# Performance work log

Measured on AMD Instinct MI355X. Metric: run time of the kernel, lower is better.

The kernel has to match this reference:

```python
import jax, jax.numpy as jnp
from jax import lax
import numpy as np

C_IN, H, W = 9, 11, 11
N_FILT = 64
N_LAYERS = 8
FC_UNITS = 64
LSTM_H = 64
N_ACTIONS = 6
B, T = 32, 128


def setup_inputs() -> dict:
    key = jax.random.key(0)
    ks = jax.random.split(key, 24)
    s = 0.05
    d = {}
    d['x'] = jax.random.normal(ks[0], (B, T, C_IN, H, W), dtype=jnp.float32)
    d['conv0_w'] = jax.random.normal(ks[1], (N_FILT, C_IN, 3, 3), dtype=jnp.float32) * s
    d['conv0_b'] = jnp.zeros((N_FILT,), jnp.float32)
    d['conv_ws'] = jax.random.normal(ks[2], (N_LAYERS - 1, N_FILT, N_FILT, 3, 3), dtype=jnp.float32) * s
    d['conv_bs'] = jnp.zeros((N_LAYERS - 1, N_FILT), jnp.float32)
    d['fc_w'] = jax.random.normal(ks[3], (FC_UNITS, N_FILT * H * W), dtype=jnp.float32) * s
    d['fc_b'] = jnp.zeros((FC_UNITS,), jnp.float32)
    d['w_ih'] = jax.random.normal(ks[4], (4 * LSTM_H, FC_UNITS), dtype=jnp.float32) * s
    d['w_hh'] = jax.random.normal(ks[5], (4 * LSTM_H, LSTM_H), dtype=jnp.float32) * s
    d['b_ih'] = jnp.zeros((4 * LSTM_H,), jnp.float32)
    d['b_hh'] = jnp.zeros((4 * LSTM_H,), jnp.float32)
    d['p1_w'] = jax.random.normal(ks[6], (128, LSTM_H), dtype=jnp.float32) * s
    d['p1_b'] = jnp.zeros((128,), jnp.float32)
    d['p2_w'] = jax.random.normal(ks[7], (N_ACTIONS, 128), dtype=jnp.float32) * s
    d['p2_b'] = jnp.zeros((N_ACTIONS,), jnp.float32)
    d['v1_w'] = jax.random.normal(ks[8], (128, LSTM_H), dtype=jnp.float32) * s
    d['v1_b'] = jnp.zeros((128,), jnp.float32)
    d['v2_w'] = jax.random.normal(ks[9], (1, 128), dtype=jnp.float32) * s
    d['v2_b'] = jnp.zeros((1,), jnp.float32)
    return d


def _conv_relu(h, w, b):
    # h: [N, C, H, W], w: [O, I, 3, 3] -> SAME padding, stride 1
    y = lax.conv_general_dilated(h, w, (1, 1), [(1, 1), (1, 1)],
                                 dimension_numbers=('NCHW', 'OIHW', 'NCHW'))
    return jax.nn.relu(y + b[None, :, None, None])


def _forward(x, conv0_w, conv0_b, conv_ws, conv_bs, fc_w, fc_b,
             w_ih, w_hh, b_ih, b_hh, p1_w, p1_b, p2_w, p2_b, v1_w, v1_b, v2_w, v2_b):
    b, t = x.shape[0], x.shape[1]
    h = x.reshape(b * t, C_IN, H, W)          # batch CNN over all frames at once
    h = _conv_relu(h, conv0_w, conv0_b)
    for i in range(N_LAYERS - 1):             # fixed small layer loop
        h = _conv_relu(h, conv_ws[i], conv_bs[i])
    h = h.reshape(b * t, N_FILT * H * W)
    feats = jax.nn.relu(h @ fc_w.T + fc_b)    # [B*T, FC_UNITS]
    feats = feats.reshape(b, t, FC_UNITS)

    # LSTM (PyTorch gate order i, f, g, o)
    def step(carry, xt):
        hprev, cprev = carry
        g = xt @ w_ih.T + hprev @ w_hh.T + b_ih + b_hh
        i_g, f_g, g_g, o_g = jnp.split(g, 4, axis=-1)
        c = jax.nn.sigmoid(f_g) * cprev + jax.nn.sigmoid(i_g) * jnp.tanh(g_g)
        hn = jax.nn.sigmoid(o_g) * jnp.tanh(c)
        return (hn, c), hn

    h0 = jnp.zeros((b, LSTM_H), feats.dtype)
    c0 = jnp.zeros((b, LSTM_H), feats.dtype)
    _, outs = lax.scan(step, (h0, c0), jnp.swapaxes(feats, 0, 1))  # [T, B, H]
    lstm_out = jnp.swapaxes(outs, 0, 1)       # [B, T, H]

    p = jax.nn.relu(lstm_out @ p1_w.T + p1_b) @ p2_w.T + p2_b  # [B, T, n_actions]
    v = jax.nn.relu(lstm_out @ v1_w.T + v1_b) @ v2_w.T + v2_b  # [B, T, 1]
    return p, v


def reference(x, conv0_w, conv0_b, conv_ws, conv_bs, fc_w, fc_b,
              w_ih, w_hh, b_ih, b_hh, p1_w, p1_b, p2_w, p2_b, v1_w, v1_b, v2_w, v2_b):
    return _forward(x, conv0_w, conv0_b, conv_ws, conv_bs, fc_w, fc_b,
                    w_ih, w_hh, b_ih, b_hh, p1_w, p1_b, p2_w, p2_b,
                    v1_w, v1_b, v2_w, v2_b)
```

## Files before the change

kernel.cpp:

```cpp
#include <hip/hip_runtime.h>
#include <hip/hip_bf16.h>

typedef __attribute__((ext_vector_type(8))) short short8;
typedef __attribute__((ext_vector_type(4))) short short4_t;
typedef __attribute__((ext_vector_type(4))) float floatx4;
typedef __attribute__((ext_vector_type(16))) float floatx16;

#define MFMA_B16(a,b,c) __builtin_amdgcn_mfma_f32_16x16x32_bf16((a),(b),(c),0,0,0)
#define MFMA32(a,b,c)   __builtin_amdgcn_mfma_f32_32x32x16_bf16((a),(b),(c),0,0,0)

__device__ __forceinline__ short f2bf(float f) {
    union { __hip_bfloat16 h; short s; } u;
    u.h = __float2bfloat16(f);
    return u.s;
}

union S8U { short4_t h[2]; short8 v; };

#define N_FRAMES 4096
#define C_IN     9
#define POS      121
#define NF       64
#define FC_K     7744
#define ISTR     20
#define FSZ      10816

#define OFF_W0    0
#define OFF_WP    18432
#define OFF_FCP   534528
#define OFF_WIHT  1525760
#define OFF_BSUM  1591296
#define OFF_ACTS  1592320
#define OFF_XG    66079744
#define OFF_HOUT  70274048

__global__ __launch_bounds__(256) void prep_kernel(
    const float* __restrict__ conv0_w, const float* __restrict__ conv_ws,
    const float* __restrict__ w_ih,
    const float* __restrict__ b_ih, const float* __restrict__ b_hh,
    short* __restrict__ w0, short* __restrict__ wpk,
    float* __restrict__ wihT, float* __restrict__ bsum)
{
    int idx = blockIdx.x*256 + threadIdx.x;
    if (idx < 9216) {
        int tap = idx >> 10; int r = idx & 1023;
        int mt = r >> 9; int o = (r >> 4) & 31; int ci = r & 15;
        int oc = mt*32 + o;
        float v = (ci < 9) ? conv0_w[(oc*9 + ci)*9 + tap] : 0.f;
        w0[idx] = f2bf(v);
        return;
    }
    idx -= 9216;
    if (idx < 258048) {
        int l = idx / 36864; int r = idx % 36864;
        int tap = r >> 12; int rr = r & 4095;
        int mt = rr >> 11;
        int ks = (rr >> 9) & 3;
        int o  = (rr >> 4) & 31;
        int ci16 = rr & 15;
        int oc = mt*32 + o;
        int ci = ks*16 + ci16;
        wpk[idx] = f2bf(conv_ws[((l*64 + oc)*64 + ci)*9 + tap]);
        return;
    }
    idx -= 258048;
    if (idx < 16384) {
        int k = idx >> 8; int g = idx & 255;
        wihT[idx] = w_ih[g*64 + k];
        return;
    }
    idx -= 16384;
    if (idx < 256) bsum[idx] = b_ih[idx] + b_hh[idx];
}

__global__ __launch_bounds__(256) void fc_transpose(
    const float* __restrict__ fc_w, short* __restrict__ fcp)
{
    __shared__ float row[FC_K];
    const int u = blockIdx.x;
    const int tid = threadIdx.x;
    const float* src = fc_w + (size_t)u*FC_K;
    for (int i = tid; i < FC_K; i += 256) row[i] = src[i];
    __syncthreads();
    short* dst = fcp + (size_t)u*FC_K;
    for (int k2 = tid; k2 < FC_K; k2 += 256) {
        int p = k2 >> 6, c = k2 & 63;
        dst[k2] = f2bf(row[c*121 + p]);
    }
}

__global__ __launch_bounds__(64, 2) void conv_stack(
    const float* __restrict__ x,
    const float* __restrict__ conv0_b,
    const float* __restrict__ conv_bs,
    const short* __restrict__ w0,
    const short* __restrict__ wpk,
    short* __restrict__ acts_out)
{
    __shared__ alignas(16) short act[FSZ];
    const int lane = threadIdx.x;
    const int n    = lane & 31;
    const int kh   = lane >> 5;
    char* actb = (char*)act;

    const short8 zero8 = {0,0,0,0,0,0,0,0};
    const floatx16 fz16 = {};

    for (int i = lane*8; i < 3392; i += 512) *(short8*)(&act[i]) = zero8;

    {
        const float* xf = x + (size_t)blockIdx.x*(C_IN*POS);
        for (int i = lane; i < C_IN*POS; i += 64) {
            int ci = i / POS;
            int p  = i - ci*POS;
            int yy = p / 11;
            int xx = p - yy*11;
            act[((yy+1)*13 + (xx+1))*ISTR + ci] = f2bf(xf[i]);
        }
    }

    floatx16 acc[2][4];
    #pragma unroll
    for (int mt=0;mt<2;mt++)
        #pragma unroll
        for (int nt=0;nt<4;nt++) acc[mt][nt] = fz16;

    int cell20[4], vbase[4], wbase[4];
    #pragma unroll
    for (int nt = 0; nt < 4; ++nt) {
        int p = nt*32 + n;
        int pc = (p <= 120) ? p : 120;
        int yy = pc / 11, xx = pc - yy*11;
        int cell = yy*13 + xx;
        cell20[nt] = cell*ISTR;
        vbase[nt]  = cell*128;
        wbase[nt]  = (cell + 14)*128;
    }

    {
        const short* w0l = w0 + n*16 + kh*8;
        #pragma unroll 1
        for (int dy = 0; dy < 3; ++dy) {
            #pragma unroll 1
            for (int dx = 0; dx < 3; ++dx) {
                const short* wt = w0l + (dy*3+dx)*1024;
                short8 a0 = *(const short8*)(wt);
                short8 a1 = *(const short8*)(wt + 512);
                const int so = (dy*13+dx)*ISTR + kh*8;
                #pragma unroll
                for (int nt=0;nt<4;nt++) {
                    const short* bp = act + cell20[nt] + so;
                    S8U t;
                    t.h[0] = *(const short4_t*)(bp);
                    t.h[1] = *(const short4_t*)(bp + 4);
                    acc[0][nt] = MFMA32(a0, t.v, acc[0][nt]);
                    acc[1][nt] = MFMA32(a1, t.v, acc[1][nt]);
                }
            }
        }
    }

    for (int i = lane*8; i < FSZ; i += 512) *(short8*)(&act[i]) = zero8;

    auto epilogue = [&](const float* bias) {
        #pragma unroll
        for (int mt=0;mt<2;mt++) {
            #pragma unroll
            for (int q=0;q<4;q++) {
                const int ch0 = mt*32 + q*8 + kh*4;
                const floatx4 bb = *(const floatx4*)(bias + ch0);
                const int soff = (((mt*4 + q + n) & 7) << 4) + kh*8;
                #pragma unroll
                for (int nt=0;nt<4;nt++) {
                    if (nt == 3 && n > 24) continue;
                    short4_t sv;
                    sv.x = f2bf(fmaxf(acc[mt][nt][q*4+0] + bb.x, 0.f));
                    sv.y = f2bf(fmaxf(acc[mt][nt][q*4+1] + bb.y, 0.f));
                    sv.z = f2bf(fmaxf(acc[mt][nt][q*4+2] + bb.z, 0.f));
                    sv.w = f2bf(fmaxf(acc[mt][nt][q*4+3] + bb.w, 0.f));
                    *(short4_t*)(actb + wbase[nt] + soff) = sv;
                }
            }
        }
        #pragma unroll
        for (int mt=0;mt<2;mt++)
            #pragma unroll
            for (int nt=0;nt<4;nt++) acc[mt][nt] = fz16;
    };

    epilogue(conv0_b);

    #pragma unroll 1
    for (int l = 1; l < 8; ++l) {
        const short* wl = wpk + (l-1)*36864 + n*16 + kh*8;
        #pragma unroll 1
        for (int dy = 0; dy < 3; ++dy) {
            #pragma unroll 1
            for (int dx = 0; dx < 3; ++dx) {
                const short* wt = wl + (dy*3+dx)*4096;
                const int sb = (dy*13+dx)*128;
                const int cu = dy*11 + dx + 4 + kh + n;
                #pragma unroll
                for (int ks = 0; ks < 4; ++ks) {
                    short8 a0 = *(const short8*)(wt + ks*512);
                    short8 a1 = *(const short8*)(wt + 2048 + ks*512);
                    const int soff = sb + (((cu + ks*2) & 7) << 4);
                    #pragma unroll
                    for (int nt=0;nt<4;nt++) {
                        short8 b = *(const short8*)(actb + vbase[nt] + soff);
                        acc[0][nt] = MFMA32(a0, b, acc[0][nt]);
                        acc[1][nt] = MFMA32(a1, b, acc[1][nt]);
                    }
                }
            }
        }
        epilogue(conv_bs + (l-1)*NF);
    }

    {
        short* dst = acts_out + (size_t)blockIdx.x*FC_K;
        #pragma unroll 1
        for (int it = 0; it < 16; ++it) {
            int q = it*64 + lane;
            if (q < 968) {
                int p = q >> 3, G = q & 7;
                int yy = p / 11, xx = p - yy*11;
                int cell = (yy+1)*13 + (xx+1);
                int slot = (G + p) & 7;
                short8 v = *(const short8*)(actb + cell*128 + slot*16);
                *(short8*)(dst + q*8) = v;
            }
        }
    }
}

__global__ __launch_bounds__(256) void fc_xg_kernel(
    const short* __restrict__ acts, const short* __restrict__ fcp,
    const float* __restrict__ fc_b, const float* __restrict__ wihT,
    const float* __restrict__ bsum, float* __restrict__ xg)
{
    __shared__ alignas(16) float red[3*64*16];
    __shared__ alignas(16) float fbuf[16*64];
    const int tid  = threadIdx.x;
    const int lane = tid & 63;
    const int w    = tid >> 6;
    const int m    = lane & 15;
    const int kg   = lane >> 4;
    const int bm   = blockIdx.x;

    const floatx4 fzero = {0.f,0.f,0.f,0.f};
    floatx4 acc[4];
    #pragma unroll
    for (int nt=0;nt<4;nt++) acc[nt] = fzero;

    const short* arow = acts + (size_t)(bm*16 + m)*FC_K + kg*8;
    const short* brow = fcp + (size_t)m*FC_K + kg*8;

    for (int kc = w; kc < 242; kc += 4) {
        short8 a = *(const short8*)(arow + kc*32);
        #pragma unroll
        for (int nt=0;nt<4;nt++) {
            short8 b = *(const short8*)(brow + (size_t)nt*16*FC_K + kc*32);
            acc[nt] = MFMA_B16(a, b, acc[nt]);
        }
    }

    if (w > 0) {
        #pragma unroll
        for (int nt=0;nt<4;nt++)
            *(floatx4*)(&red[((w-1)*64 + lane)*16 + nt*4]) = acc[nt];
    }
    __syncthreads();
    if (w == 0) {
        #pragma unroll
        for (int nt=0;nt<4;nt++)
            for (int j=0;j<3;j++)
                acc[nt] += *(const floatx4*)(&red[(j*64 + lane)*16 + nt*4]);
        #pragma unroll
        for (int nt=0;nt<4;nt++) {
            int unit = nt*16 + m;
            float bias = fc_b[unit];
            int fr = kg*4;
            fbuf[(fr+0)*NF + unit] = fmaxf(acc[nt].x + bias, 0.f);
            fbuf[(fr+1)*NF + unit] = fmaxf(acc[nt].y + bias, 0.f);
            fbuf[(fr+2)*NF + unit] = fmaxf(acc[nt].z + bias, 0.f);
            fbuf[(fr+3)*NF + unit] = fmaxf(acc[nt].w + bias, 0.f);
        }
    }
    __syncthreads();

    {
        const int g = tid;
        float a[16];
        float bs = bsum[g];
        #pragma unroll
        for (int i=0;i<16;i++) a[i] = bs;
        for (int k=0;k<64;k++) {
            float wk = wihT[k*256 + g];
            #pragma unroll
            for (int i=0;i<16;i++) a[i] += fbuf[i*64 + k] * wk;
        }
        float* xo = xg + (size_t)(bm*16)*256 + g;
        #pragma unroll
        for (int i=0;i<16;i++) xo[i*256] = a[i];
    }
}

__device__ __forceinline__ float sigmf_(float v){
    return __builtin_amdgcn_rcpf(1.f + __expf(-v));
}
__device__ __forceinline__ float tanhf_(float v){
    return 1.f - 2.f*__builtin_amdgcn_rcpf(__expf(2.f*v) + 1.f);
}

__global__ __launch_bounds__(128) void lstm_kernel(
    const float* __restrict__ xg, const float* __restrict__ whh,
    float* __restrict__ hout)
{
    __shared__ alignas(16) float hbuf[64];
    __shared__ alignas(16) float gbuf[256];
    const int t = threadIdx.x;
    const int b = blockIdx.x;

    float4 w0v[16], w1v[16];
    #pragma unroll
    for (int k=0;k<16;k++) w0v[k] = *(const float4*)(whh + t*64 + k*4);
    #pragma unroll
    for (int k=0;k<16;k++) w1v[k] = *(const float4*)(whh + (t+128)*64 + k*4);

    float c = 0.f;
    if (t < 64) hbuf[t] = 0.f;
    __syncthreads();

    const float* xr = xg + (size_t)(b*128)*256;
    float nA = xr[t];
    float nB = xr[t+128];

    for (int ts=0; ts<128; ++ts) {
        float aA = nA, aB = nB;
        if (ts + 1 < 128) {
            const float* xn = xr + (ts+1)*256;
            nA = xn[t];
            nB = xn[t+128];
        }
        #pragma unroll
        for (int k=0;k<16;k++) {
            float4 hv = *(const float4*)(&hbuf[k*4]);
            aA += hv.x*w0v[k].x + hv.y*w0v[k].y + hv.z*w0v[k].z + hv.w*w0v[k].w;
            aB += hv.x*w1v[k].x + hv.y*w1v[k].y + hv.z*w1v[k].z + hv.w*w1v[k].w;
        }
        gbuf[t] = aA;
        gbuf[t+128] = aB;
        __syncthreads();
        if (t < 64) {
            float ig = sigmf_(gbuf[t]);
            float fg = sigmf_(gbuf[64+t]);
            float gg = tanhf_(gbuf[128+t]);
            float og = sigmf_(gbuf[192+t]);
            c = fg*c + ig*gg;
            float h = og*tanhf_(c);
            hbuf[t] = h;
            hout[(b*128+ts)*64 + t] = h;
        }
        __syncthreads();
    }
}

__global__ __launch_bounds__(64) void heads_kernel(
    const float* __restrict__ hout,
    const float* __restrict__ p1w, const float* __restrict__ p1b,
    const float* __restrict__ p2w, const float* __restrict__ p2b,
    const float* __restrict__ v1w, const float* __restrict__ v1b,
    const float* __restrict__ v2w, const float* __restrict__ v2b,
    float* __restrict__ out)
{
    __shared__ alignas(16) float hbuf[64];
    __shared__ alignas(16) float a1[128];
    __shared__ alignas(16) float a2[128];
    const int lane = threadIdx.x;
    for (int fi=0; fi<4; ++fi) {
        const int f = blockIdx.x*4 + fi;
        hbuf[lane] = hout[f*64 + lane];
        __syncthreads();
        #pragma unroll
        for (int uu=0; uu<2; ++uu) {
            const int u = lane + uu*64;
            float s1 = p1b[u], s2 = v1b[u];
            const float4* wp1 = (const float4*)(p1w + u*64);
            const float4* wv1 = (const float4*)(v1w + u*64);
            #pragma unroll
            for (int k=0;k<16;k++) {
                float4 h4 = *(const float4*)(&hbuf[k*4]);
                float4 w4 = wp1[k];
                s1 += h4.x*w4.x + h4.y*w4.y + h4.z*w4.z + h4.w*w4.w;
                float4 q4 = wv1[k];
                s2 += h4.x*q4.x + h4.y*q4.y + h4.z*q4.z + h4.w*q4.w;
            }
            a1[u] = fmaxf(s1, 0.f);
            a2[u] = fmaxf(s2, 0.f);
        }
        __syncthreads();
        if (lane < 6) {
            float s = p2b[lane];
            const float* wr = p2w + lane*128;
            #pragma unroll
            for (int j=0;j<128;j++) s += a1[j]*wr[j];
            out[f*6 + lane] = s;
        }
        if (lane == 6) {
            float s = v2b[0];
            #pragma unroll
            for (int j=0;j<128;j++) s += a2[j]*v2w[j];
            out[24576 + f] = s;
        }
        __syncthreads();
    }
}

extern "C" void kernel_launch(void* const* d_in, const int* in_sizes, int n_in,
                              void* d_out, int out_size, void* d_ws, size_t ws_size,
                              hipStream_t stream) {
    const float* x       = (const float*)d_in[0];
    const float* conv0_w = (const float*)d_in[1];
    const float* conv0_b = (const float*)d_in[2];
    const float* conv_ws = (const float*)d_in[3];
    const float* conv_bs = (const float*)d_in[4];
    const float* fc_w    = (const float*)d_in[5];
    const float* fc_b    = (const float*)d_in[6];
    const float* w_ih    = (const float*)d_in[7];
    const float* w_hh    = (const float*)d_in[8];
    const float* b_ih    = (const float*)d_in[9];
    const float* b_hh    = (const float*)d_in[10];
    const float* p1_w    = (const float*)d_in[11];
    const float* p1_b    = (const float*)d_in[12];
    const float* p2_w    = (const float*)d_in[13];
    const float* p2_b    = (const float*)d_in[14];
    const float* v1_w    = (const float*)d_in[15];
    const float* v1_b    = (const float*)d_in[16];
    const float* v2_w    = (const float*)d_in[17];
    const float* v2_b    = (const float*)d_in[18];
    float* out = (float*)d_out;

    char* ws = (char*)d_ws;
    short* w0    = (short*)(ws + OFF_W0);
    short* wpk   = (short*)(ws + OFF_WP);
    short* fcp   = (short*)(ws + OFF_FCP);
    float* wihT  = (float*)(ws + OFF_WIHT);
    float* bsum  = (float*)(ws + OFF_BSUM);
    short* acts  = (short*)(ws + OFF_ACTS);
    float* xgb   = (float*)(ws + OFF_XG);
    float* hout  = (float*)(ws + OFF_HOUT);

    prep_kernel<<<1109, 256, 0, stream>>>(conv0_w, conv_ws, w_ih, b_ih, b_hh,
                                          w0, wpk, wihT, bsum);
    fc_transpose<<<64, 256, 0, stream>>>(fc_w, fcp);
    conv_stack<<<N_FRAMES, 64, 0, stream>>>(x, conv0_b, conv_bs, w0, wpk, acts);
    fc_xg_kernel<<<256, 256, 0, stream>>>(acts, fcp, fc_b, wihT, bsum, xgb);
    lstm_kernel<<<32, 128, 0, stream>>>(xgb, w_hh, hout);
    heads_kernel<<<1024, 64, 0, stream>>>(hout, p1_w, p1_b, p2_w, p2_b,
                                          v1_w, v1_b, v2_w, v2_b, out);
}
```

Before: 549.2 us.

## Split conv_stack positions across two wavefronts per frame block

Each frame's conv stack now runs on two wavefronts (128 threads), each computing half of the spatial position tiles, instead of one wavefront doing all four. Accumulator registers per thread drop by half, which allows higher occupancy (launch bounds raised to 3 blocks) and more latency hiding. In exchange, block-wide barriers are added around every layer epilogue, and each wave still loads the full weight tiles, so weight traffic per MFMA doubles.

```diff
diff --git a/kernel.cpp b/kernel.cpp
--- a/kernel.cpp
+++ b/kernel.cpp
@@ -89,7 +89,7 @@
     }
 }
 
-__global__ __launch_bounds__(64, 2) void conv_stack(
+__global__ __launch_bounds__(128, 3) void conv_stack(
     const float* __restrict__ x,
     const float* __restrict__ conv0_b,
     const float* __restrict__ conv_bs,
@@ -98,7 +98,9 @@
     short* __restrict__ acts_out)
 {
     __shared__ alignas(16) short act[FSZ];
-    const int lane = threadIdx.x;
+    const int tid  = threadIdx.x;
+    const int lane = tid & 63;
+    const int wv   = tid >> 6;
     const int n    = lane & 31;
     const int kh   = lane >> 5;
     char* actb = (char*)act;
@@ -106,11 +108,12 @@
     const short8 zero8 = {0,0,0,0,0,0,0,0};
     const floatx16 fz16 = {};
 
-    for (int i = lane*8; i < 3392; i += 512) *(short8*)(&act[i]) = zero8;
+    for (int i = tid*8; i < 3392; i += 1024) *(short8*)(&act[i]) = zero8;
+    __syncthreads();
 
     {
         const float* xf = x + (size_t)blockIdx.x*(C_IN*POS);
-        for (int i = lane; i < C_IN*POS; i += 64) {
+        for (int i = tid; i < C_IN*POS; i += 128) {
             int ci = i / POS;
             int p  = i - ci*POS;
             int yy = p / 11;
@@ -118,24 +121,26 @@
             act[((yy+1)*13 + (xx+1))*ISTR + ci] = f2bf(xf[i]);
         }
     }
-
-    floatx16 acc[2][4];
+    __syncthreads();
+
+    floatx16 acc[2][2];
     #pragma unroll
     for (int mt=0;mt<2;mt++)
         #pragma unroll
-        for (int nt=0;nt<4;nt++) acc[mt][nt] = fz16;
-
-    int cell20[4], vbase[4], wbase[4];
+        for (int j=0;j<2;j++) acc[mt][j] = fz16;
+
+    int cell20[2], vbase[2], wbase[2];
     #pragma unroll
-    for (int nt = 0; nt < 4; ++nt) {
-        int p = nt*32 + n;
+    for (int j = 0; j < 2; ++j) {
+        int p = (wv*2 + j)*32 + n;
         int pc = (p <= 120) ? p : 120;
         int yy = pc / 11, xx = pc - yy*11;
         int cell = yy*13 + xx;
-        cell20[nt] = cell*ISTR;
-        vbase[nt]  = cell*128;
-        wbase[nt]  = (cell + 14)*128;
-    }
+        cell20[j] = cell*ISTR;
+        vbase[j]  = cell*128;
+        wbase[j]  = (cell + 14)*128;
+    }
+    const bool tail = (wv == 1) && (n > 24);
 
     {
         const short* w0l = w0 + n*16 + kh*8;
@@ -148,21 +153,23 @@
                 short8 a1 = *(const short8*)(wt + 512);
                 const int so = (dy*13+dx)*ISTR + kh*8;
                 #pragma unroll
-                for (int nt=0;nt<4;nt++) {
-                    const short* bp = act + cell20[nt] + so;
+                for (int j=0;j<2;j++) {
+                    const short* bp = act + cell20[j] + so;
                     S8U t;
                     t.h[0] = *(const short4_t*)(bp);
                     t.h[1] = *(const short4_t*)(bp + 4);
-                    acc[0][nt] = MFMA32(a0, t.v, acc[0][nt]);
-                    acc[1][nt] = MFMA32(a1, t.v, acc[1][nt]);
+                    acc[0][j] = MFMA32(a0, t.v, acc[0][j]);
+                    acc[1][j] = MFMA32(a1, t.v, acc[1][j]);
                 }
             }
         }
     }
 
-    for (int i = lane*8; i < FSZ; i += 512) *(short8*)(&act[i]) = zero8;
+    __syncthreads();
+    for (int i = tid*8; i < FSZ; i += 1024) *(short8*)(&act[i]) = zero8;
 
     auto epilogue = [&](const float* bias) {
+        __syncthreads();
         #pragma unroll
         for (int mt=0;mt<2;mt++) {
             #pragma unroll
@@ -171,21 +178,22 @@
                 const floatx4 bb = *(const floatx4*)(bias + ch0);
                 const int soff = (((mt*4 + q + n) & 7) << 4) + kh*8;
                 #pragma unroll
-                for (int nt=0;nt<4;nt++) {
-                    if (nt == 3 && n > 24) continue;
+                for (int j=0;j<2;j++) {
+                    if (j == 1 && tail) continue;
                     short4_t sv;
-                    sv.x = f2bf(fmaxf(acc[mt][nt][q*4+0] + bb.x, 0.f));
-                    sv.y = f2bf(fmaxf(acc[mt][nt][q*4+1] + bb.y, 0.f));
-                    sv.z = f2bf(fmaxf(acc[mt][nt][q*4+2] + bb.z, 0.f));
-                    sv.w = f2bf(fmaxf(acc[mt][nt][q*4+3] + bb.w, 0.f));
-                    *(short4_t*)(actb + wbase[nt] + soff) = sv;
+                    sv.x = f2bf(fmaxf(acc[mt][j][q*4+0] + bb.x, 0.f));
+                    sv.y = f2bf(fmaxf(acc[mt][j][q*4+1] + bb.y, 0.f));
+                    sv.z = f2bf(fmaxf(acc[mt][j][q*4+2] + bb.z, 0.f));
+                    sv.w = f2bf(fmaxf(acc[mt][j][q*4+3] + bb.w, 0.f));
+                    *(short4_t*)(actb + wbase[j] + soff) = sv;
                 }
             }
         }
         #pragma unroll
         for (int mt=0;mt<2;mt++)
             #pragma unroll
-            for (int nt=0;nt<4;nt++) acc[mt][nt] = fz16;
+            for (int j=0;j<2;j++) acc[mt][j] = fz16;
+        __syncthreads();
     };
 
     epilogue(conv0_b);
@@ -206,10 +214,10 @@
                     short8 a1 = *(const short8*)(wt + 2048 + ks*512);
                     const int soff = sb + (((cu + ks*2) & 7) << 4);
                     #pragma unroll
-                    for (int nt=0;nt<4;nt++) {
-                        short8 b = *(const short8*)(actb + vbase[nt] + soff);
-                        acc[0][nt] = MFMA32(a0, b, acc[0][nt]);
-                        acc[1][nt] = MFMA32(a1, b, acc[1][nt]);
+                    for (int j=0;j<2;j++) {
+                        short8 b = *(const short8*)(actb + vbase[j] + soff);
+                        acc[0][j] = MFMA32(a0, b, acc[0][j]);
+                        acc[1][j] = MFMA32(a1, b, acc[1][j]);
                     }
                 }
             }
@@ -220,8 +228,8 @@
     {
         short* dst = acts_out + (size_t)blockIdx.x*FC_K;
         #pragma unroll 1
-        for (int it = 0; it < 16; ++it) {
-            int q = it*64 + lane;
+        for (int it = 0; it < 8; ++it) {
+            int q = it*128 + tid;
             if (q < 968) {
                 int p = q >> 3, G = q & 7;
                 int yy = p / 11, xx = p - yy*11;
@@ -454,7 +462,7 @@
     prep_kernel<<<1109, 256, 0, stream>>>(conv0_w, conv_ws, w_ih, b_ih, b_hh,
                                           w0, wpk, wihT, bsum);
     fc_transpose<<<64, 256, 0, stream>>>(fc_w, fcp);
-    conv_stack<<<N_FRAMES, 64, 0, stream>>>(x, conv0_b, conv_bs, w0, wpk, acts);
+    conv_stack<<<N_FRAMES, 128, 0, stream>>>(x, conv0_b, conv_bs, w0, wpk, acts);
     fc_xg_kernel<<<256, 256, 0, stream>>>(acts, fcp, fc_b, wihT, bsum, xgb);
     lstm_kernel<<<32, 128, 0, stream>>>(xgb, w_hh, hout);
     heads_kernel<<<1024, 64, 0, stream>>>(hout, p1_w, p1_b, p2_w, p2_b,
```

Result: faster. 528.6 us (-3.8%).
